# Kernel tuning notes

Measured on AMD Instinct MI355X. Metric: run time of the kernel, lower is better.

## Reference

```python
import jax, jax.numpy as jnp
import numpy as np

HIDDEN = 3584
N_HEADS = 28
N_KV = 4
HEAD_DIM = 128
MROPE = [16, 24, 24]          # sums to HEAD_DIM // 2
W_BITS = 4                    # per-output-channel symmetric weight fake-quant
A_BITS = 8                    # per-tensor symmetric activation fake-quant
ROPE_THETA = 1000000.0
B, S = 1, 2048


def fake_quant(x, bits, axis=None):
    """Symmetric uniform fake-quant with straight-through estimator."""
    qmax = 2.0 ** (bits - 1) - 1
    if axis is None:
        s = jnp.max(jnp.abs(x)) / qmax
    else:
        s = jnp.max(jnp.abs(x), axis=axis, keepdims=True) / qmax
    s = jnp.maximum(s, 1e-8)
    dq = jnp.clip(jnp.round(x / s), -qmax - 1.0, qmax) * s
    return x + jax.lax.stop_gradient(dq - x)


def quant_linear(x, w, b):
    """QuantLinear: fake-quant activations (per-tensor) and weights (per out-channel)."""
    xq = fake_quant(x, A_BITS)
    wq = fake_quant(w, W_BITS, axis=1)        # w: [out, in]
    y = xq @ wq.T
    return y + b if b is not None else y


def rotate_half(x):
    x1, x2 = jnp.split(x, 2, axis=-1)
    return jnp.concatenate([-x2, x1], axis=-1)


def apply_multimodal_rope(q, k, cos, sin):
    """cos/sin: (3, b, s, head_dim). Interleave t/h/w sections per mrope_section."""
    splits = np.cumsum([m * 2 for m in MROPE])[:-1]

    def mix(t):
        parts = jnp.split(t, splits, axis=-1)
        return jnp.concatenate([parts[i][i % 3] for i in range(len(parts))], axis=-1)[:, None]  # (b,1,s,hd)

    c, s_ = mix(cos), mix(sin)
    q_emb = q * c + rotate_half(q) * s_
    k_emb = k * c + rotate_half(k) * s_
    return q_emb, k_emb


def setup_inputs() -> dict:
    key = jax.random.key(0)
    ks = jax.random.split(key, 8)
    hidden_states = jax.random.normal(ks[0], (B, S, HIDDEN), dtype=jnp.float32)
    # realistic rotary embeddings, broadcast over the 3 mrope axes (text: all equal)
    inv_freq = 1.0 / (ROPE_THETA ** (np.arange(0, HEAD_DIM, 2, dtype=np.float32) / HEAD_DIM))
    pos = np.arange(S, dtype=np.float32)
    freqs = pos[:, None] * inv_freq[None, :]                  # (S, hd/2)
    emb = np.concatenate([freqs, freqs], axis=-1)             # (S, hd)
    cos = jnp.asarray(np.broadcast_to(np.cos(emb)[None, None], (3, B, S, HEAD_DIM)).copy())
    sin = jnp.asarray(np.broadcast_to(np.sin(emb)[None, None], (3, B, S, HEAD_DIM)).copy())
    sc = 0.02
    wq = jax.random.normal(ks[1], (HIDDEN, HIDDEN), dtype=jnp.float32) * sc
    bq = jax.random.normal(ks[2], (HIDDEN,), dtype=jnp.float32) * sc
    wk = jax.random.normal(ks[3], (N_KV * HEAD_DIM, HIDDEN), dtype=jnp.float32) * sc
    bk = jax.random.normal(ks[4], (N_KV * HEAD_DIM,), dtype=jnp.float32) * sc
    wv = jax.random.normal(ks[5], (N_KV * HEAD_DIM, HIDDEN), dtype=jnp.float32) * sc
    bv = jax.random.normal(ks[6], (N_KV * HEAD_DIM,), dtype=jnp.float32) * sc
    wo = jax.random.normal(ks[7], (HIDDEN, HIDDEN), dtype=jnp.float32) * sc
    return {"hidden_states": hidden_states, "cos": cos, "sin": sin,
            "wq": wq, "bq": bq, "wk": wk, "bk": bk, "wv": wv, "bv": bv, "wo": wo}


def reference(hidden_states, cos, sin, wq, bq, wk, bk, wv, bv, wo):
    b, s, _ = hidden_states.shape
    q = quant_linear(hidden_states, wq, bq).reshape(b, s, N_HEADS, HEAD_DIM).transpose(0, 2, 1, 3)
    k = quant_linear(hidden_states, wk, bk).reshape(b, s, N_KV, HEAD_DIM).transpose(0, 2, 1, 3)
    v = quant_linear(hidden_states, wv, bv).reshape(b, s, N_KV, HEAD_DIM).transpose(0, 2, 1, 3)
    q, k = apply_multimodal_rope(q, k, cos, sin)
    g = N_HEADS // N_KV
    k = jnp.repeat(k, g, axis=1)   # repeat_kv
    v = jnp.repeat(v, g, axis=1)
    scores = jnp.einsum('bhqd,bhkd->bhqk', q, k) / np.float32(np.sqrt(HEAD_DIM))
    causal = jnp.tril(jnp.ones((s, s), dtype=bool))
    scores = jnp.where(causal[None, None], scores, jnp.finfo(scores.dtype).min)
    p = jax.nn.softmax(scores, axis=-1)
    attn = jnp.einsum('bhqk,bhkd->bhqd', p, v)
    attn = attn.transpose(0, 2, 1, 3).reshape(b, s, N_HEADS * HEAD_DIM)
    return quant_linear(attn, wo, None)
```

## Files before the change

kernel.cpp:

```cpp
#include <hip/hip_runtime.h>
#include <stdint.h>


#define S_LEN 2048
#define HID   3584
#define NH    28
#define NKV   4
#define HD    128
#define GQA   7
#define KD    3584

typedef signed char i8;
typedef unsigned short u16;
typedef __attribute__((ext_vector_type(4))) int      v4i;
typedef __attribute__((ext_vector_type(4))) float    v4f;
typedef __attribute__((ext_vector_type(8))) _Float16 f16x8;
typedef __attribute__((ext_vector_type(4))) float    f32x4;

#define QK_SCALE   4096.0f
#define S_UNSCALE  5.9604644775390625e-8f
#define V_SCALE    64.0f
#define P_SCALE    16384.0f
#define O_UNSCALE  9.5367431640625e-7f

#define GLOAD_LDS(g, l) __builtin_amdgcn_global_load_lds( \
    (__attribute__((address_space(1))) void*)(g),          \
    (__attribute__((address_space(3))) void*)(l), 16, 0, 0)

static __device__ __forceinline__ u16 f16bits(_Float16 h) {
  u16 u; __builtin_memcpy(&u, &h, 2); return u;
}
static __device__ __forceinline__ void splitf16(float x, u16& hb, u16& lb) {
  _Float16 h = (_Float16)x;
  float r = x - (float)h;
  _Float16 l = (_Float16)r;
  hb = f16bits(h); lb = f16bits(l);
}

__global__ void k_zero(float* p) {
  if (threadIdx.x < 8) p[threadIdx.x] = 0.0f;
}

__global__ void k_absmax(const float* __restrict__ x, long long n, unsigned* __restrict__ out) {
  long long i0 = ((long long)blockIdx.x * blockDim.x + threadIdx.x) * 4;
  long long stride = (long long)gridDim.x * blockDim.x * 4;
  float m = 0.0f;
  for (long long i = i0; i < n; i += stride) {
    f32x4 v = *(const f32x4*)(x + i);
    m = fmaxf(m, fmaxf(fmaxf(fabsf(v.x), fabsf(v.y)), fmaxf(fabsf(v.z), fabsf(v.w))));
  }
  #pragma unroll
  for (int o = 32; o > 0; o >>= 1) m = fmaxf(m, __shfl_xor(m, o, 64));
  __shared__ float sm[4];
  if ((threadIdx.x & 63) == 0) sm[threadIdx.x >> 6] = m;
  __syncthreads();
  if (threadIdx.x == 0) {
    m = fmaxf(fmaxf(sm[0], sm[1]), fmaxf(sm[2], sm[3]));
    atomicMax(out, __float_as_uint(m));
  }
}

__global__ void k_quant_act(const float* __restrict__ x, i8* __restrict__ q,
                            const unsigned* __restrict__ amax, long long n) {
  float s = fmaxf(__uint_as_float(*amax) / 127.0f, 1e-8f);
  long long i = ((long long)blockIdx.x * blockDim.x + threadIdx.x) * 4;
  if (i >= n) return;
  f32x4 v = *(const f32x4*)(x + i);
  char4 c;
  c.x = (char)fminf(fmaxf(rintf(v.x / s), -128.0f), 127.0f);
  c.y = (char)fminf(fmaxf(rintf(v.y / s), -128.0f), 127.0f);
  c.z = (char)fminf(fmaxf(rintf(v.z / s), -128.0f), 127.0f);
  c.w = (char)fminf(fmaxf(rintf(v.w / s), -128.0f), 127.0f);
  *(char4*)(q + i) = c;
}

__global__ void k_quant_w(const float* __restrict__ w, i8* __restrict__ wq,
                          float* __restrict__ sw) {
  const int row = blockIdx.x;
  const float2* wr = (const float2*)(w + (long long)row * KD);
  float2 v[7];
  float m = 0.0f;
  #pragma unroll
  for (int j = 0; j < 7; j++) {
    v[j] = wr[threadIdx.x + 256 * j];
    m = fmaxf(m, fmaxf(fabsf(v[j].x), fabsf(v[j].y)));
  }
  #pragma unroll
  for (int o = 32; o > 0; o >>= 1) m = fmaxf(m, __shfl_xor(m, o, 64));
  __shared__ float sm[4];
  if ((threadIdx.x & 63) == 0) sm[threadIdx.x >> 6] = m;
  __syncthreads();
  const float mm = fmaxf(fmaxf(sm[0], sm[1]), fmaxf(sm[2], sm[3]));
  const float s = fmaxf(mm / 7.0f, 1e-8f);
  if (threadIdx.x == 0) sw[row] = s;
  u16* o = (u16*)(wq + (long long)row * KD);
  #pragma unroll
  for (int j = 0; j < 7; j++) {
    const int c0 = (int)fminf(fmaxf(rintf(v[j].x / s), -8.0f), 7.0f);
    const int c1 = (int)fminf(fmaxf(rintf(v[j].y / s), -8.0f), 7.0f);
    o[threadIdx.x + 256 * j] = (u16)((c0 & 0xff) | ((c1 & 0xff) << 8));
  }
}

__global__ __launch_bounds__(256, 3) void k_gemm(
    const i8* __restrict__ Aq,
    const i8* __restrict__ W0, const i8* __restrict__ W1, const i8* __restrict__ W2,
    const float* __restrict__ sw0, const float* __restrict__ sw1, const float* __restrict__ sw2,
    const float* __restrict__ b0, const float* __restrict__ b1, const float* __restrict__ b2,
    const float* __restrict__ cosb, const float* __restrict__ sinb,
    const unsigned* __restrict__ amax_slot,
    u16* __restrict__ qhi, u16* __restrict__ qlo,
    u16* __restrict__ khi, u16* __restrict__ klo,
    u16* __restrict__ vthi, u16* __restrict__ vtlo,
    float* __restrict__ outO, int kind) {
  __shared__ i8 As[128 * 64];
  __shared__ i8 Bs[128 * 64];
  const int tid = threadIdx.x, wid = tid >> 6, lane = tid & 63;

  const int q8 = (int)gridDim.x >> 3;
  const int orig = blockIdx.x;
  const int wgid = (orig & 7) * q8 + (orig >> 3);
  const int ct = wgid >> 4;
  const int mb = wgid & 15;

  const i8* Bw; const float* sw; const float* bias; int epi; int nbase;
  if (kind == 1)      { Bw = W0; sw = sw0; bias = nullptr; epi = 3; nbase = ct * 128; }
  else if (ct < 28)   { Bw = W0; sw = sw0; bias = b0;      epi = 0; nbase = ct * 128; }
  else if (ct < 32)   { Bw = W1; sw = sw1; bias = b1;      epi = 1; nbase = (ct - 28) * 128; }
  else                { Bw = W2; sw = sw2; bias = b2;      epi = 2; nbase = (ct - 32) * 128; }

  const float s_a = fmaxf(__uint_as_float(*amax_slot) / 127.0f, 1e-8f);

  v4i acc[2][8];
  #pragma unroll
  for (int a = 0; a < 2; a++)
    #pragma unroll
    for (int b = 0; b < 8; b++) acc[a][b] = (v4i)(0);

  const long long arow0 = (long long)mb * 128 * KD;
  const long long brow0 = (long long)nbase * KD;

  for (int kt = 0; kt < KD / 64; ++kt) {
    const int k0 = kt * 64;
    #pragma unroll
    for (int j = 0; j < 2; j++) {
      const int c = tid + 256 * j;
      const int r = c >> 2, seg = c & 3;
      const int so = (seg ^ ((r >> 1) & 3)) << 4;
      GLOAD_LDS(Aq + arow0 + (long long)r * KD + k0 + so, As + c * 16);
      GLOAD_LDS(Bw + brow0 + (long long)r * KD + k0 + so, Bs + c * 16);
    }
    __syncthreads();
    v4i af[2];
    #pragma unroll
    for (int mt = 0; mt < 2; mt++) {
      const int rl = wid * 32 + mt * 16 + (lane & 15);
      af[mt] = *(const v4i*)(As + rl * 64 + ((((lane >> 4)) ^ ((rl >> 1) & 3)) << 4));
    }
    #pragma unroll
    for (int nt = 0; nt < 8; nt++) {
      const int rb = nt * 16 + (lane & 15);
      const v4i bfr = *(const v4i*)(Bs + rb * 64 + ((((lane >> 4)) ^ ((rb >> 1) & 3)) << 4));
      acc[0][nt] = __builtin_amdgcn_mfma_i32_16x16x64_i8(af[0], bfr, acc[0][nt], 0, 0, 0);
      acc[1][nt] = __builtin_amdgcn_mfma_i32_16x16x64_i8(af[1], bfr, acc[1][nt], 0, 0, 0);
    }
    __syncthreads();
  }

  float y[2][8][4];
  #pragma unroll
  for (int mt = 0; mt < 2; mt++)
    #pragma unroll
    for (int nt = 0; nt < 8; nt++) {
      const int n = nbase + nt * 16 + (lane & 15);
      const float sc = s_a * sw[n];
      const float bb = bias ? bias[n] : 0.0f;
      #pragma unroll
      for (int r = 0; r < 4; r++) y[mt][nt][r] = sc * (float)acc[mt][nt][r] + bb;
    }

  if (epi == 3) {
    #pragma unroll
    for (int mt = 0; mt < 2; mt++)
      #pragma unroll
      for (int r = 0; r < 4; r++) {
        const int m_ = mb * 128 + wid * 32 + mt * 16 + ((lane >> 4) << 2) + r;
        #pragma unroll
        for (int nt = 0; nt < 8; nt++)
          outO[(long long)m_ * HID + ct * 128 + nt * 16 + (lane & 15)] = y[mt][nt][r];
      }
  } else if (epi == 2) {
    const int gkv = ct - 32;
    #pragma unroll
    for (int mt = 0; mt < 2; mt++)
      #pragma unroll
      for (int nt = 0; nt < 8; nt++) {
        const int d = nt * 16 + (lane & 15);
        const int mbase = mb * 128 + wid * 32 + mt * 16 + ((lane >> 4) << 2);
        ushort4 hv, lv;
        #pragma unroll
        for (int r = 0; r < 4; r++)
          splitf16(y[mt][nt][r] * V_SCALE, ((u16*)&hv)[r], ((u16*)&lv)[r]);
        const long long o = ((long long)(gkv * HD + d)) * S_LEN + mbase;
        *(ushort4*)(vthi + o) = hv;
        *(ushort4*)(vtlo + o) = lv;
      }
  } else {
    const int head = (epi == 0) ? ct : (ct - 28);
    u16* oh = (epi == 0) ? qhi : khi;
    u16* ol = (epi == 0) ? qlo : klo;
    const float qs = (epi == 0) ? 0.08838834764831845f * QK_SCALE : QK_SCALE;
    #pragma unroll
    for (int mt = 0; mt < 2; mt++)
      #pragma unroll
      for (int r = 0; r < 4; r++) {
        const int m_ = mb * 128 + wid * 32 + mt * 16 + ((lane >> 4) << 2) + r;
        #pragma unroll
        for (int nt = 0; nt < 8; nt++) {
          const int d = nt * 16 + (lane & 15);
          const int sec = (d < 32) ? 0 : ((d < 80) ? 1 : 2);
          const long long ci = ((long long)sec * S_LEN + m_) * HD + d;
          const float c = cosb[ci], s = sinb[ci];
          const float part = (nt < 4) ? -y[mt][nt + 4][r] : y[mt][nt - 4][r];
          const float e = (y[mt][nt][r] * c + part * s) * qs;
          const long long o = ((long long)head * S_LEN + m_) * HD + d;
          splitf16(e, oh[o], ol[o]);
        }
      }
  }
}

__global__ __launch_bounds__(256, 2) void k_attn(
    const u16* __restrict__ qhi, const u16* __restrict__ qlo,
    const u16* __restrict__ khi, const u16* __restrict__ klo,
    const u16* __restrict__ vthi, const u16* __restrict__ vtlo,
    float* __restrict__ attn, unsigned* __restrict__ amax) {
  const int h = blockIdx.x;
  const int qt = (int)gridDim.y - 1 - (int)blockIdx.y;
  const int g = h / GQA;
  const int tid = threadIdx.x, wid = tid >> 6, lane = tid & 63;

  __shared__ u16 KH[64 * 128], KL[64 * 128];
  __shared__ u16 VH[128 * 64], VL[128 * 64];
  u16* PH = KH + wid * (32 * 64);
  u16* PL = KL + wid * (32 * 64);

  f16x8 qh[2][4], ql[2][4];
  #pragma unroll
  for (int mt = 0; mt < 2; mt++) {
    const int row = qt * 128 + wid * 32 + mt * 16 + (lane & 15);
    const long long base = ((long long)h * S_LEN + row) * HD + ((lane >> 4) << 3);
    #pragma unroll
    for (int kc = 0; kc < 4; kc++) {
      qh[mt][kc] = *(const f16x8*)(qhi + base + kc * 32);
      ql[mt][kc] = *(const f16x8*)(qlo + base + kc * 32);
    }
  }

  v4f O[2][8];
  #pragma unroll
  for (int a = 0; a < 2; a++)
    #pragma unroll
    for (int b = 0; b < 8; b++) O[a][b] = (v4f)(0.0f);
  float mrun[2][4], lsum[2][4];
  #pragma unroll
  for (int a = 0; a < 2; a++)
    #pragma unroll
    for (int r = 0; r < 4; r++) { mrun[a][r] = -1e30f; lsum[a][r] = 0.0f; }

  const int qmaxw = qt * 128 + wid * 32 + 31;
  const int ktiles = 2 * qt + 2;
  for (int kt = 0; kt < ktiles; ++kt) {
    const int s0 = kt * 64;
    #pragma unroll
    for (int j = 0; j < 4; j++) {
      const int c = tid + 256 * j;
      const int r = c >> 4, seg = c & 15;
      const long long gb = ((long long)g * S_LEN + s0 + r) * HD + ((seg ^ (r & 7)) << 3);
      GLOAD_LDS(khi + gb, (i8*)KH + c * 16);
      GLOAD_LDS(klo + gb, (i8*)KL + c * 16);
    }
    #pragma unroll
    for (int j = 0; j < 4; j++) {
      const int c = tid + 256 * j;
      const int d = c >> 3, seg = c & 7;
      const long long gb = ((long long)(g * HD + d)) * S_LEN + s0 + ((seg ^ (d & 7)) << 3);
      GLOAD_LDS(vthi + gb, (i8*)VH + c * 16);
      GLOAD_LDS(vtlo + gb, (i8*)VL + c * 16);
    }
    __syncthreads();

    const bool active = (s0 <= qmaxw);
    v4f S[2][4];
    if (active) {
      #pragma unroll
      for (int a = 0; a < 2; a++)
        #pragma unroll
        for (int b = 0; b < 4; b++) S[a][b] = (v4f)(0.0f);
      __builtin_amdgcn_s_setprio(1);
      #pragma unroll
      for (int kc = 0; kc < 4; kc++) {
        #pragma unroll
        for (int nt = 0; nt < 4; nt++) {
          const int rk = nt * 16 + (lane & 15);
          const int ch = kc * 4 + (lane >> 4);
          const int idx = rk * 128 + ((ch ^ (rk & 7)) << 3);
          const f16x8 kh = *(const f16x8*)(KH + idx);
          const f16x8 kl = *(const f16x8*)(KL + idx);
          #pragma unroll
          for (int mt = 0; mt < 2; mt++) {
            S[mt][nt] = __builtin_amdgcn_mfma_f32_16x16x32_f16(qh[mt][kc], kh, S[mt][nt], 0, 0, 0);
            S[mt][nt] = __builtin_amdgcn_mfma_f32_16x16x32_f16(qh[mt][kc], kl, S[mt][nt], 0, 0, 0);
            S[mt][nt] = __builtin_amdgcn_mfma_f32_16x16x32_f16(ql[mt][kc], kh, S[mt][nt], 0, 0, 0);
          }
        }
      }
      __builtin_amdgcn_s_setprio(0);
      #pragma unroll
      for (int mt = 0; mt < 2; mt++)
        #pragma unroll
        for (int r = 0; r < 4; r++) {
          const int q_g = qt * 128 + wid * 32 + mt * 16 + ((lane >> 4) << 2) + r;
          float sv[4];
          float tm = -1e30f;
          #pragma unroll
          for (int nt = 0; nt < 4; nt++) {
            const int kp = s0 + nt * 16 + (lane & 15);
            sv[nt] = (kp <= q_g) ? S[mt][nt][r] * S_UNSCALE : -1e30f;
            tm = fmaxf(tm, sv[nt]);
          }
          tm = fmaxf(tm, __shfl_xor(tm, 1, 64));
          tm = fmaxf(tm, __shfl_xor(tm, 2, 64));
          tm = fmaxf(tm, __shfl_xor(tm, 4, 64));
          tm = fmaxf(tm, __shfl_xor(tm, 8, 64));
          const float nm = fmaxf(mrun[mt][r], tm);
          const float rs = __expf(mrun[mt][r] - nm);
          mrun[mt][r] = nm;
          float ps = 0.0f;
          #pragma unroll
          for (int nt = 0; nt < 4; nt++) {
            const float p = (sv[nt] > -1e29f) ? __expf(sv[nt] - nm) : 0.0f;
            ps += p;
            S[mt][nt][r] = p;
          }
          ps += __shfl_xor(ps, 1, 64);
          ps += __shfl_xor(ps, 2, 64);
          ps += __shfl_xor(ps, 4, 64);
          ps += __shfl_xor(ps, 8, 64);
          if (rs != 1.0f) {
            lsum[mt][r] = lsum[mt][r] * rs + ps;
            #pragma unroll
            for (int nt = 0; nt < 8; nt++) O[mt][nt][r] *= rs;
          } else {
            lsum[mt][r] += ps;
          }
        }
    }
    __syncthreads();

    if (active) {
      #pragma unroll
      for (int mt = 0; mt < 2; mt++)
        #pragma unroll
        for (int r = 0; r < 4; r++) {
          const int q_l = mt * 16 + ((lane >> 4) << 2) + r;
          #pragma unroll
          for (int nt = 0; nt < 4; nt++) {
            const int kp_l = nt * 16 + (lane & 15);
            const int ch = kp_l >> 3;
            const int idx = q_l * 64 + ((ch ^ (q_l & 7)) << 3) + (kp_l & 7);
            splitf16(S[mt][nt][r] * P_SCALE, PH[idx], PL[idx]);
          }
        }
      #pragma unroll
      for (int kc = 0; kc < 2; kc++) {
        f16x8 pa[2], pb[2];
        #pragma unroll
        for (int mt = 0; mt < 2; mt++) {
          const int rq = mt * 16 + (lane & 15);
          const int ch = kc * 4 + (lane >> 4);
          const int idx = rq * 64 + ((ch ^ (rq & 7)) << 3);
          pa[mt] = *(const f16x8*)&PH[idx];
          pb[mt] = *(const f16x8*)&PL[idx];
        }
        __builtin_amdgcn_s_setprio(1);
        #pragma unroll
        for (int nt = 0; nt < 8; nt++) {
          const int rd = nt * 16 + (lane & 15);
          const int ch = kc * 4 + (lane >> 4);
          const int idx = rd * 64 + ((ch ^ (rd & 7)) << 3);
          const f16x8 vh = *(const f16x8*)(VH + idx);
          const f16x8 vl = *(const f16x8*)(VL + idx);
          #pragma unroll
          for (int mt = 0; mt < 2; mt++) {
            O[mt][nt] = __builtin_amdgcn_mfma_f32_16x16x32_f16(pa[mt], vh, O[mt][nt], 0, 0, 0);
            O[mt][nt] = __builtin_amdgcn_mfma_f32_16x16x32_f16(pb[mt], vh, O[mt][nt], 0, 0, 0);
            O[mt][nt] = __builtin_amdgcn_mfma_f32_16x16x32_f16(pa[mt], vl, O[mt][nt], 0, 0, 0);
          }
        }
        __builtin_amdgcn_s_setprio(0);
      }
    }
    __syncthreads();
  }

  float am = 0.0f;
  #pragma unroll
  for (int mt = 0; mt < 2; mt++)
    #pragma unroll
    for (int r = 0; r < 4; r++) {
      const int q_g = qt * 128 + wid * 32 + mt * 16 + ((lane >> 4) << 2) + r;
      const float inv = O_UNSCALE / lsum[mt][r];
      #pragma unroll
      for (int nt = 0; nt < 8; nt++) {
        const float val = O[mt][nt][r] * inv;
        attn[(long long)q_g * HID + h * HD + nt * 16 + (lane & 15)] = val;
        am = fmaxf(am, fabsf(val));
      }
    }
  am = fmaxf(am, __shfl_xor(am, 1, 64));
  am = fmaxf(am, __shfl_xor(am, 2, 64));
  am = fmaxf(am, __shfl_xor(am, 4, 64));
  am = fmaxf(am, __shfl_xor(am, 8, 64));
  am = fmaxf(am, __shfl_xor(am, 16, 64));
  am = fmaxf(am, __shfl_xor(am, 32, 64));
  if (lane == 0) atomicMax(amax, __float_as_uint(am));
}

extern "C" void kernel_launch(void* const* d_in, const int* in_sizes, int n_in,
                              void* d_out, int out_size, void* d_ws, size_t ws_size,
                              hipStream_t stream) {
  const float* hidden = (const float*)d_in[0];
  const float* cosb   = (const float*)d_in[1];
  const float* sinb   = (const float*)d_in[2];
  const float* wq     = (const float*)d_in[3];
  const float* bq     = (const float*)d_in[4];
  const float* wk     = (const float*)d_in[5];
  const float* bk     = (const float*)d_in[6];
  const float* wv     = (const float*)d_in[7];
  const float* bv     = (const float*)d_in[8];
  const float* wo     = (const float*)d_in[9];
  float* out = (float*)d_out;

  char* w = (char*)d_ws;
  size_t off = 0;
  auto alloc = [&](size_t bytes) -> void* {
    void* p = w + off;
    off += (bytes + 255) & ~(size_t)255;
    return p;
  };
  unsigned* scal = (unsigned*)alloc(256);
  i8* xq8   = (i8*)alloc((size_t)S_LEN * KD);
  i8* wq8   = (i8*)alloc((size_t)HID * KD);
  i8* wk8   = (i8*)alloc((size_t)NKV * HD * KD);
  i8* wv8   = (i8*)alloc((size_t)NKV * HD * KD);
  i8* wo8   = (i8*)alloc((size_t)HID * KD);
  float* swq = (float*)alloc(HID * 4);
  float* swk = (float*)alloc(NKV * HD * 4);
  float* swv = (float*)alloc(NKV * HD * 4);
  float* swo = (float*)alloc(HID * 4);
  u16* qhi_  = (u16*)alloc((size_t)NH * S_LEN * HD * 2);
  u16* qlo_  = (u16*)alloc((size_t)NH * S_LEN * HD * 2);
  u16* khi_  = (u16*)alloc((size_t)NKV * S_LEN * HD * 2);
  u16* klo_  = (u16*)alloc((size_t)NKV * S_LEN * HD * 2);
  u16* vthi_ = (u16*)alloc((size_t)NKV * S_LEN * HD * 2);
  u16* vtlo_ = (u16*)alloc((size_t)NKV * S_LEN * HD * 2);
  float* attnb = (float*)alloc((size_t)S_LEN * HID * 4);

  const long long nact = (long long)S_LEN * KD;

  k_zero<<<1, 64, 0, stream>>>((float*)scal);
  k_absmax<<<1024, 256, 0, stream>>>(hidden, nact, scal + 0);
  k_quant_w<<<HID, 256, 0, stream>>>(wq, wq8, swq);
  k_quant_w<<<NKV * HD, 256, 0, stream>>>(wk, wk8, swk);
  k_quant_w<<<NKV * HD, 256, 0, stream>>>(wv, wv8, swv);
  k_quant_w<<<HID, 256, 0, stream>>>(wo, wo8, swo);
  k_quant_act<<<(int)(nact / 4 / 256), 256, 0, stream>>>(hidden, xq8, scal + 0, nact);

  k_gemm<<<dim3(36 * 16), 256, 0, stream>>>(
      xq8, wq8, wk8, wv8, swq, swk, swv, bq, bk, bv, cosb, sinb, scal + 0,
      qhi_, qlo_, khi_, klo_, vthi_, vtlo_, nullptr, 0);

  k_attn<<<dim3(NH, 16), 256, 0, stream>>>(qhi_, qlo_, khi_, klo_, vthi_, vtlo_,
                                           attnb, scal + 1);

  k_quant_act<<<(int)(nact / 4 / 256), 256, 0, stream>>>(attnb, xq8, scal + 1, nact);

  k_gemm<<<dim3(28 * 16), 256, 0, stream>>>(
      xq8, wo8, nullptr, nullptr, swo, nullptr, nullptr, nullptr, nullptr, nullptr,
      nullptr, nullptr, scal + 1,
      nullptr, nullptr, nullptr, nullptr, nullptr, nullptr, out, 1);
}
```

Measured before the change: 639.3 us.

## Double-buffer K/V tiles and pair causal q-tiles per attention block

The attention kernel now stages K/V tiles into a double-buffered LDS region so the next tile's global-to-LDS load overlaps compute on the current one. Each block processes two query tiles (qt and 15-qt), which balances causal work across blocks, and a swizzled 1D grid of 224 blocks replaces the 28x16 grid. LDS doubles, so launch bounds drop to one block per CU, trading occupancy for overlap and load balance.

New measurement: 558.1 us. 12.7% less time.

```diff
diff --git a/kernel.cpp b/kernel.cpp
--- a/kernel.cpp
+++ b/kernel.cpp
@@ -230,194 +230,216 @@
   }
 }
 
-__global__ __launch_bounds__(256, 2) void k_attn(
+__global__ __launch_bounds__(256, 1) void k_attn(
     const u16* __restrict__ qhi, const u16* __restrict__ qlo,
     const u16* __restrict__ khi, const u16* __restrict__ klo,
     const u16* __restrict__ vthi, const u16* __restrict__ vtlo,
     float* __restrict__ attn, unsigned* __restrict__ amax) {
-  const int h = blockIdx.x;
-  const int qt = (int)gridDim.y - 1 - (int)blockIdx.y;
+  const int orig = blockIdx.x;
+  const int nchunk = (int)gridDim.x >> 3;
+  const int swz = (orig & 7) * nchunk + (orig >> 3);
+  const int h = swz >> 3;
+  const int p = swz & 7;
   const int g = h / GQA;
   const int tid = threadIdx.x, wid = tid >> 6, lane = tid & 63;
 
-  __shared__ u16 KH[64 * 128], KL[64 * 128];
-  __shared__ u16 VH[128 * 64], VL[128 * 64];
-  u16* PH = KH + wid * (32 * 64);
-  u16* PL = KL + wid * (32 * 64);
-
-  f16x8 qh[2][4], ql[2][4];
-  #pragma unroll
-  for (int mt = 0; mt < 2; mt++) {
-    const int row = qt * 128 + wid * 32 + mt * 16 + (lane & 15);
-    const long long base = ((long long)h * S_LEN + row) * HD + ((lane >> 4) << 3);
-    #pragma unroll
-    for (int kc = 0; kc < 4; kc++) {
-      qh[mt][kc] = *(const f16x8*)(qhi + base + kc * 32);
-      ql[mt][kc] = *(const f16x8*)(qlo + base + kc * 32);
+  __shared__ u16 KH[2][64 * 128], KL[2][64 * 128];
+  __shared__ u16 VH[2][128 * 64], VL[2][128 * 64];
+
+#define STAGE(b, t) do {                                                        \
+    const int s0_ = (t) * 64;                                                   \
+    _Pragma("unroll")                                                           \
+    for (int j_ = 0; j_ < 4; j_++) {                                            \
+      const int c_ = tid + 256 * j_;                                            \
+      const int r_ = c_ >> 4, sg_ = c_ & 15;                                    \
+      const long long gb_ = ((long long)g * S_LEN + s0_ + r_) * HD +            \
+                            ((sg_ ^ (r_ & 7)) << 3);                            \
+      GLOAD_LDS(khi + gb_, (i8*)KH[(b)] + c_ * 16);                             \
+      GLOAD_LDS(klo + gb_, (i8*)KL[(b)] + c_ * 16);                             \
+    }                                                                           \
+    _Pragma("unroll")                                                           \
+    for (int j_ = 0; j_ < 4; j_++) {                                            \
+      const int c_ = tid + 256 * j_;                                            \
+      const int d_ = c_ >> 3, sg_ = c_ & 7;                                     \
+      const long long gb_ = ((long long)(g * HD + d_)) * S_LEN + s0_ +          \
+                            ((sg_ ^ (d_ & 7)) << 3);                            \
+      GLOAD_LDS(vthi + gb_, (i8*)VH[(b)] + c_ * 16);                            \
+      GLOAD_LDS(vtlo + gb_, (i8*)VL[(b)] + c_ * 16);                            \
+    }                                                                           \
+  } while (0)
+
+  float am = 0.0f;
+
+  for (int pass = 0; pass < 2; ++pass) {
+    const int qt = pass ? p : 15 - p;
+    const int ktn = 2 * qt + 2;
+
+    STAGE(0, 0);
+
+    f16x8 qh[2][4], ql[2][4];
+    #pragma unroll
+    for (int mt = 0; mt < 2; mt++) {
+      const int row = qt * 128 + wid * 32 + mt * 16 + (lane & 15);
+      const long long base = ((long long)h * S_LEN + row) * HD + ((lane >> 4) << 3);
+      #pragma unroll
+      for (int kc = 0; kc < 4; kc++) {
+        qh[mt][kc] = *(const f16x8*)(qhi + base + kc * 32);
+        ql[mt][kc] = *(const f16x8*)(qlo + base + kc * 32);
+      }
     }
-  }
-
-  v4f O[2][8];
-  #pragma unroll
-  for (int a = 0; a < 2; a++)
-    #pragma unroll
-    for (int b = 0; b < 8; b++) O[a][b] = (v4f)(0.0f);
-  float mrun[2][4], lsum[2][4];
-  #pragma unroll
-  for (int a = 0; a < 2; a++)
-    #pragma unroll
-    for (int r = 0; r < 4; r++) { mrun[a][r] = -1e30f; lsum[a][r] = 0.0f; }
-
-  const int qmaxw = qt * 128 + wid * 32 + 31;
-  const int ktiles = 2 * qt + 2;
-  for (int kt = 0; kt < ktiles; ++kt) {
-    const int s0 = kt * 64;
-    #pragma unroll
-    for (int j = 0; j < 4; j++) {
-      const int c = tid + 256 * j;
-      const int r = c >> 4, seg = c & 15;
-      const long long gb = ((long long)g * S_LEN + s0 + r) * HD + ((seg ^ (r & 7)) << 3);
-      GLOAD_LDS(khi + gb, (i8*)KH + c * 16);
-      GLOAD_LDS(klo + gb, (i8*)KL + c * 16);
-    }
-    #pragma unroll
-    for (int j = 0; j < 4; j++) {
-      const int c = tid + 256 * j;
-      const int d = c >> 3, seg = c & 7;
-      const long long gb = ((long long)(g * HD + d)) * S_LEN + s0 + ((seg ^ (d & 7)) << 3);
-      GLOAD_LDS(vthi + gb, (i8*)VH + c * 16);
-      GLOAD_LDS(vtlo + gb, (i8*)VL + c * 16);
-    }
+
+    v4f O[2][8];
+    #pragma unroll
+    for (int a = 0; a < 2; a++)
+      #pragma unroll
+      for (int b = 0; b < 8; b++) O[a][b] = (v4f)(0.0f);
+    float mrun[2][4], lsum[2][4];
+    #pragma unroll
+    for (int a = 0; a < 2; a++)
+      #pragma unroll
+      for (int r = 0; r < 4; r++) { mrun[a][r] = -1e30f; lsum[a][r] = 0.0f; }
+
+    const int qmaxw = qt * 128 + wid * 32 + 31;
     __syncthreads();
 
-    const bool active = (s0 <= qmaxw);
-    v4f S[2][4];
-    if (active) {
-      #pragma unroll
-      for (int a = 0; a < 2; a++)
-        #pragma unroll
-        for (int b = 0; b < 4; b++) S[a][b] = (v4f)(0.0f);
-      __builtin_amdgcn_s_setprio(1);
-      #pragma unroll
-      for (int kc = 0; kc < 4; kc++) {
-        #pragma unroll
-        for (int nt = 0; nt < 4; nt++) {
-          const int rk = nt * 16 + (lane & 15);
-          const int ch = kc * 4 + (lane >> 4);
-          const int idx = rk * 128 + ((ch ^ (rk & 7)) << 3);
-          const f16x8 kh = *(const f16x8*)(KH + idx);
-          const f16x8 kl = *(const f16x8*)(KL + idx);
+    for (int s = 0; s < ktn; ++s) {
+      const int cur = s & 1;
+      const int s0 = s * 64;
+      u16* PH = KH[cur] + wid * 2048;
+      u16* PL = KL[cur] + wid * 2048;
+
+      if (s + 1 < ktn) STAGE(cur ^ 1, s + 1);
+
+      const bool active = (s0 <= qmaxw);
+      v4f S[2][4];
+      if (active) {
+        #pragma unroll
+        for (int a = 0; a < 2; a++)
           #pragma unroll
-          for (int mt = 0; mt < 2; mt++) {
-            S[mt][nt] = __builtin_amdgcn_mfma_f32_16x16x32_f16(qh[mt][kc], kh, S[mt][nt], 0, 0, 0);
-            S[mt][nt] = __builtin_amdgcn_mfma_f32_16x16x32_f16(qh[mt][kc], kl, S[mt][nt], 0, 0, 0);
-            S[mt][nt] = __builtin_amdgcn_mfma_f32_16x16x32_f16(ql[mt][kc], kh, S[mt][nt], 0, 0, 0);
-          }
-        }
-      }
-      __builtin_amdgcn_s_setprio(0);
-      #pragma unroll
-      for (int mt = 0; mt < 2; mt++)
-        #pragma unroll
-        for (int r = 0; r < 4; r++) {
-          const int q_g = qt * 128 + wid * 32 + mt * 16 + ((lane >> 4) << 2) + r;
-          float sv[4];
-          float tm = -1e30f;
+          for (int b = 0; b < 4; b++) S[a][b] = (v4f)(0.0f);
+        __builtin_amdgcn_s_setprio(1);
+        #pragma unroll
+        for (int kc = 0; kc < 4; kc++) {
           #pragma unroll
           for (int nt = 0; nt < 4; nt++) {
-            const int kp = s0 + nt * 16 + (lane & 15);
-            sv[nt] = (kp <= q_g) ? S[mt][nt][r] * S_UNSCALE : -1e30f;
-            tm = fmaxf(tm, sv[nt]);
-          }
-          tm = fmaxf(tm, __shfl_xor(tm, 1, 64));
-          tm = fmaxf(tm, __shfl_xor(tm, 2, 64));
-          tm = fmaxf(tm, __shfl_xor(tm, 4, 64));
-          tm = fmaxf(tm, __shfl_xor(tm, 8, 64));
-          const float nm = fmaxf(mrun[mt][r], tm);
-          const float rs = __expf(mrun[mt][r] - nm);
-          mrun[mt][r] = nm;
-          float ps = 0.0f;
-          #pragma unroll
-          for (int nt = 0; nt < 4; nt++) {
-            const float p = (sv[nt] > -1e29f) ? __expf(sv[nt] - nm) : 0.0f;
-            ps += p;
-            S[mt][nt][r] = p;
-          }
-          ps += __shfl_xor(ps, 1, 64);
-          ps += __shfl_xor(ps, 2, 64);
-          ps += __shfl_xor(ps, 4, 64);
-          ps += __shfl_xor(ps, 8, 64);
-          if (rs != 1.0f) {
-            lsum[mt][r] = lsum[mt][r] * rs + ps;
+            const int rk = nt * 16 + (lane & 15);
+            const int ch = kc * 4 + (lane >> 4);
+            const int idx = rk * 128 + ((ch ^ (rk & 7)) << 3);
+            const f16x8 kh = *(const f16x8*)(KH[cur] + idx);
+            const f16x8 kl = *(const f16x8*)(KL[cur] + idx);
             #pragma unroll
-            for (int nt = 0; nt < 8; nt++) O[mt][nt][r] *= rs;
-          } else {
-            lsum[mt][r] += ps;
-          }
-        }
-    }
-    __syncthreads();
-
-    if (active) {
-      #pragma unroll
-      for (int mt = 0; mt < 2; mt++)
-        #pragma unroll
-        for (int r = 0; r < 4; r++) {
-          const int q_l = mt * 16 + ((lane >> 4) << 2) + r;
-          #pragma unroll
-          for (int nt = 0; nt < 4; nt++) {
-            const int kp_l = nt * 16 + (lane & 15);
-            const int ch = kp_l >> 3;
-            const int idx = q_l * 64 + ((ch ^ (q_l & 7)) << 3) + (kp_l & 7);
-            splitf16(S[mt][nt][r] * P_SCALE, PH[idx], PL[idx]);
-          }
-        }
-      #pragma unroll
-      for (int kc = 0; kc < 2; kc++) {
-        f16x8 pa[2], pb[2];
-        #pragma unroll
-        for (int mt = 0; mt < 2; mt++) {
-          const int rq = mt * 16 + (lane & 15);
-          const int ch = kc * 4 + (lane >> 4);
-          const int idx = rq * 64 + ((ch ^ (rq & 7)) << 3);
-          pa[mt] = *(const f16x8*)&PH[idx];
-          pb[mt] = *(const f16x8*)&PL[idx];
-        }
-        __builtin_amdgcn_s_setprio(1);
-        #pragma unroll
-        for (int nt = 0; nt < 8; nt++) {
-          const int rd = nt * 16 + (lane & 15);
-          const int ch = kc * 4 + (lane >> 4);
-          const int idx = rd * 64 + ((ch ^ (rd & 7)) << 3);
-          const f16x8 vh = *(const f16x8*)(VH + idx);
-          const f16x8 vl = *(const f16x8*)(VL + idx);
-          #pragma unroll
-          for (int mt = 0; mt < 2; mt++) {
-            O[mt][nt] = __builtin_amdgcn_mfma_f32_16x16x32_f16(pa[mt], vh, O[mt][nt], 0, 0, 0);
-            O[mt][nt] = __builtin_amdgcn_mfma_f32_16x16x32_f16(pb[mt], vh, O[mt][nt], 0, 0, 0);
-            O[mt][nt] = __builtin_amdgcn_mfma_f32_16x16x32_f16(pa[mt], vl, O[mt][nt], 0, 0, 0);
+            for (int mt = 0; mt < 2; mt++) {
+              S[mt][nt] = __builtin_amdgcn_mfma_f32_16x16x32_f16(qh[mt][kc], kh, S[mt][nt], 0, 0, 0);
+              S[mt][nt] = __builtin_amdgcn_mfma_f32_16x16x32_f16(qh[mt][kc], kl, S[mt][nt], 0, 0, 0);
+              S[mt][nt] = __builtin_amdgcn_mfma_f32_16x16x32_f16(ql[mt][kc], kh, S[mt][nt], 0, 0, 0);
+            }
           }
         }
         __builtin_amdgcn_s_setprio(0);
-      }
+        #pragma unroll
+        for (int mt = 0; mt < 2; mt++)
+          #pragma unroll
+          for (int r = 0; r < 4; r++) {
+            const int q_g = qt * 128 + wid * 32 + mt * 16 + ((lane >> 4) << 2) + r;
+            float sv[4];
+            float tm = -1e30f;
+            #pragma unroll
+            for (int nt = 0; nt < 4; nt++) {
+              const int kp = s0 + nt * 16 + (lane & 15);
+              sv[nt] = (kp <= q_g) ? S[mt][nt][r] * S_UNSCALE : -1e30f;
+              tm = fmaxf(tm, sv[nt]);
+            }
+            tm = fmaxf(tm, __shfl_xor(tm, 1, 64));
+            tm = fmaxf(tm, __shfl_xor(tm, 2, 64));
+            tm = fmaxf(tm, __shfl_xor(tm, 4, 64));
+            tm = fmaxf(tm, __shfl_xor(tm, 8, 64));
+            const float nm = fmaxf(mrun[mt][r], tm);
+            const float rs = __expf(mrun[mt][r] - nm);
+            mrun[mt][r] = nm;
+            float ps = 0.0f;
+            #pragma unroll
+            for (int nt = 0; nt < 4; nt++) {
+              const float pv = (sv[nt] > -1e29f) ? __expf(sv[nt] - nm) : 0.0f;
+              ps += pv;
+              S[mt][nt][r] = pv;
+            }
+            ps += __shfl_xor(ps, 1, 64);
+            ps += __shfl_xor(ps, 2, 64);
+            ps += __shfl_xor(ps, 4, 64);
+            ps += __shfl_xor(ps, 8, 64);
+            if (rs != 1.0f) {
+              lsum[mt][r] = lsum[mt][r] * rs + ps;
+              #pragma unroll
+              for (int nt = 0; nt < 8; nt++) O[mt][nt][r] *= rs;
+            } else {
+              lsum[mt][r] += ps;
+            }
+          }
+      }
+      __syncthreads();
+
+      if (active) {
+        #pragma unroll
+        for (int mt = 0; mt < 2; mt++)
+          #pragma unroll
+          for (int r = 0; r < 4; r++) {
+            const int q_l = mt * 16 + ((lane >> 4) << 2) + r;
+            #pragma unroll
+            for (int nt = 0; nt < 4; nt++) {
+              const int kp_l = nt * 16 + (lane & 15);
+              const int ch = kp_l >> 3;
+              const int idx = q_l * 64 + ((ch ^ (q_l & 7)) << 3) + (kp_l & 7);
+              splitf16(S[mt][nt][r] * P_SCALE, PH[idx], PL[idx]);
+            }
+          }
+        #pragma unroll
+        for (int kc = 0; kc < 2; kc++) {
+          f16x8 pa[2], pb[2];
+          #pragma unroll
+          for (int mt = 0; mt < 2; mt++) {
+            const int rq = mt * 16 + (lane & 15);
+            const int ch = kc * 4 + (lane >> 4);
+            const int idx = rq * 64 + ((ch ^ (rq & 7)) << 3);
+            pa[mt] = *(const f16x8*)&PH[idx];
+            pb[mt] = *(const f16x8*)&PL[idx];
+          }
+          __builtin_amdgcn_s_setprio(1);
+          #pragma unroll
+          for (int nt = 0; nt < 8; nt++) {
+            const int rd = nt * 16 + (lane & 15);
+            const int ch = kc * 4 + (lane >> 4);
+            const int idx = rd * 64 + ((ch ^ (rd & 7)) << 3);
+            const f16x8 vh = *(const f16x8*)(VH[cur] + idx);
+            const f16x8 vl = *(const f16x8*)(VL[cur] + idx);
+            #pragma unroll
+            for (int mt = 0; mt < 2; mt++) {
+              O[mt][nt] = __builtin_amdgcn_mfma_f32_16x16x32_f16(pa[mt], vh, O[mt][nt], 0, 0, 0);
+              O[mt][nt] = __builtin_amdgcn_mfma_f32_16x16x32_f16(pb[mt], vh, O[mt][nt], 0, 0, 0);
+              O[mt][nt] = __builtin_amdgcn_mfma_f32_16x16x32_f16(pa[mt], vl, O[mt][nt], 0, 0, 0);
+            }
+          }
+          __builtin_amdgcn_s_setprio(0);
+        }
+      }
+      __syncthreads();
     }
-    __syncthreads();
-  }
-
-  float am = 0.0f;
-  #pragma unroll
-  for (int mt = 0; mt < 2; mt++)
-    #pragma unroll
-    for (int r = 0; r < 4; r++) {
-      const int q_g = qt * 128 + wid * 32 + mt * 16 + ((lane >> 4) << 2) + r;
-      const float inv = O_UNSCALE / lsum[mt][r];
-      #pragma unroll
-      for (int nt = 0; nt < 8; nt++) {
-        const float val = O[mt][nt][r] * inv;
-        attn[(long long)q_g * HID + h * HD + nt * 16 + (lane & 15)] = val;
-        am = fmaxf(am, fabsf(val));
-      }
-    }
+
+    #pragma unroll
+    for (int mt = 0; mt < 2; mt++)
+      #pragma unroll
+      for (int r = 0; r < 4; r++) {
+        const int q_g = qt * 128 + wid * 32 + mt * 16 + ((lane >> 4) << 2) + r;
+        const float inv = O_UNSCALE / lsum[mt][r];
+        #pragma unroll
+        for (int nt = 0; nt < 8; nt++) {
+          const float val = O[mt][nt][r] * inv;
+          attn[(long long)q_g * HID + h * HD + nt * 16 + (lane & 15)] = val;
+          am = fmaxf(am, fabsf(val));
+        }
+      }
+  }
+#undef STAGE
+
   am = fmaxf(am, __shfl_xor(am, 1, 64));
   am = fmaxf(am, __shfl_xor(am, 2, 64));
   am = fmaxf(am, __shfl_xor(am, 4, 64));
@@ -481,7 +503,7 @@
       xq8, wq8, wk8, wv8, swq, swk, swv, bq, bk, bv, cosb, sinb, scal + 0,
       qhi_, qlo_, khi_, klo_, vthi_, vtlo_, nullptr, 0);
 
-  k_attn<<<dim3(NH, 16), 256, 0, stream>>>(qhi_, qlo_, khi_, klo_, vthi_, vtlo_,
+  k_attn<<<dim3(NH * 8), 256, 0, stream>>>(qhi_, qlo_, khi_, klo_, vthi_, vtlo_,
                                            attnb, scal + 1);
 
   k_quant_act<<<(int)(nact / 4 / 256), 256, 0, stream>>>(attnb, xq8, scal + 1, nact);
```
